# Optimization experiments

Measured on AMD Instinct MI355X. Metric: run time of the kernel, lower is better.

## Reference

```python
import jax, jax.numpy as jnp
import numpy as np

NUM_HEADS = 16
HEAD_DIM = 128
ROPE_BASE = 10000.0


def _rotate_half(x):
    x1, x2 = jnp.split(x, 2, axis=-1)
    return jnp.concatenate([-x2, x1], axis=-1)


def setup_inputs() -> dict:
    key = jax.random.key(0)
    ks = jax.random.split(key, 6)
    B, S, H = 2, 2048, 2048
    hidden_states = jax.random.normal(ks[0], (B, S, H), dtype=jnp.float32)
    # causal additive mask: 0 on/below diagonal, large negative above
    causal = jnp.tril(jnp.ones((S, S), dtype=bool))
    attention_mask = jnp.where(causal, 0.0, -1e9).astype(jnp.float32)[None, None]
    position_ids = jnp.broadcast_to(jnp.arange(S, dtype=jnp.int64), (B, S))
    sc = 1.0 / np.sqrt(H)
    Wq = jax.random.normal(ks[1], (H, H), dtype=jnp.float32) * sc
    Wk = jax.random.normal(ks[2], (H, H), dtype=jnp.float32) * sc
    Wv = jax.random.normal(ks[3], (H, H), dtype=jnp.float32) * sc
    Wo = jax.random.normal(ks[4], (H, H), dtype=jnp.float32) * sc
    return {"hidden_states": hidden_states, "attention_mask": attention_mask,
            "position_ids": position_ids, "Wq": Wq, "Wk": Wk, "Wv": Wv, "Wo": Wo}


def reference(hidden_states, attention_mask, position_ids, Wq, Wk, Wv, Wo):
    B, S, H = hidden_states.shape
    nH, hd = NUM_HEADS, HEAD_DIM
    # projections (torch Linear: x @ W.T)
    q = (hidden_states @ Wq.T).reshape(B, S, nH, hd).transpose(0, 2, 1, 3)  # [B,nH,S,hd]
    k = (hidden_states @ Wk.T).reshape(B, S, nH, hd).transpose(0, 2, 1, 3)
    v = (hidden_states @ Wv.T).reshape(B, S, nH, hd).transpose(0, 2, 1, 3)
    # rotary embeddings: cos/sin cache over positions, duplicated to full head_dim
    inv_freq = 1.0 / (ROPE_BASE ** (jnp.arange(0, hd, 2, dtype=jnp.float32) / hd))  # [hd/2]
    t = jnp.arange(S, dtype=jnp.float32)
    freqs = jnp.outer(t, inv_freq)                       # [S, hd/2]
    emb = jnp.concatenate([freqs, freqs], axis=-1)       # [S, hd]
    cos = jnp.cos(emb)[position_ids][:, None]            # [B,1,S,hd]
    sin = jnp.sin(emb)[position_ids][:, None]
    q = q * cos + _rotate_half(q) * sin
    k = k * cos + _rotate_half(k) * sin
    # eager attention
    scores = jnp.einsum('bhqd,bhkd->bhqk', q, k) / np.sqrt(hd).astype(np.float32)
    scores = scores + attention_mask
    attn = jax.nn.softmax(scores, axis=-1)
    out = jnp.einsum('bhqk,bhkd->bhqd', attn, v)         # [B,nH,S,hd]
    out = out.transpose(0, 2, 1, 3).reshape(B, S, H)
    return out @ Wo.T
```

## Files before the change

kernel.cpp:

```cpp
#include <hip/hip_runtime.h>
#include <cstdint>
#include <cstddef>

#define NH    16
#define HD    128
#define SEQ   2048
#define HID   2048
#define BATCH 2
#define MTOT  (BATCH*SEQ)

#define SCALE 0.08838834764831845f
#define L2E   1.4426950408889634f
#define KSCL  (0.08838834764831845f * 1.4426950408889634f)

typedef __bf16 bf16x8 __attribute__((ext_vector_type(8)));
typedef float  floatx4 __attribute__((ext_vector_type(4)));

__device__ __forceinline__ unsigned short f2bf(float f) {
  union { float f; unsigned u; } v; v.f = f;
  unsigned u = v.u;
  return (unsigned short)((u + 0x7FFFu + ((u >> 16) & 1u)) >> 16);
}
__device__ __forceinline__ float bf2f(unsigned short h) {
  union { unsigned u; float f; } v; v.u = ((unsigned)h) << 16; return v.f;
}

__device__ __forceinline__ void gld16(const unsigned short* g, unsigned short* l) {
  auto gp = reinterpret_cast<const __attribute__((address_space(1))) void*>(
      reinterpret_cast<uintptr_t>(g));
  auto lp = reinterpret_cast<__attribute__((address_space(3))) void*>(
      reinterpret_cast<uintptr_t>(l));
  __builtin_amdgcn_global_load_lds(gp, lp, 16, 0, 0);
}

__global__ void cvt_f32_bf16(const float* __restrict__ src,
                             unsigned short* __restrict__ dst, int n4) {
  int i = blockIdx.x * blockDim.x + threadIdx.x;
  if (i >= n4) return;
  float4 v = reinterpret_cast<const float4*>(src)[i];
  ushort4 o;
  o.x = f2bf(v.x); o.y = f2bf(v.y); o.z = f2bf(v.z); o.w = f2bf(v.w);
  reinterpret_cast<ushort4*>(dst)[i] = o;
}

__global__ void rope_table(float2* __restrict__ tab) {
  int idx = blockIdx.x * blockDim.x + threadIdx.x;
  if (idx >= SEQ * 64) return;
  int pos = idx >> 6, i = idx & 63;
  double freq = pow(10000.0, -(double)(2 * i) / 128.0);
  double th = (double)pos * freq;
  tab[idx] = make_float2((float)cos(th), (float)sin(th));
}

__global__ void rope_qk(unsigned short* __restrict__ Q,
                        unsigned short* __restrict__ Kk,
                        const float2* __restrict__ tab) {
  int idx = blockIdx.x * blockDim.x + threadIdx.x;
  if (idx >= BATCH * NH * SEQ * 64) return;
  int i  = idx & 63;
  int s  = (idx >> 6) & (SEQ - 1);
  int bh = idx >> 17;
  float2 cs = tab[s * 64 + i];
  size_t base = ((size_t)bh * SEQ + s) * HD;
  float qa = bf2f(Q[base + i]), qb = bf2f(Q[base + i + 64]);
  Q[base + i]      = f2bf(qa * cs.x - qb * cs.y);
  Q[base + i + 64] = f2bf(qb * cs.x + qa * cs.y);
  float ka = bf2f(Kk[base + i]), kb = bf2f(Kk[base + i + 64]);
  Kk[base + i]      = f2bf(ka * cs.x - kb * cs.y);
  Kk[base + i + 64] = f2bf(kb * cs.x + ka * cs.y);
}

__device__ __forceinline__ void gemm_core(const unsigned short* __restrict__ A,
                                          const unsigned short* __restrict__ B,
                                          int K, int mBase, int nBase,
                                          unsigned short* As, unsigned short* Bs,
                                          floatx4 acc[4][4]) {
  int tid  = threadIdx.x;
  int wave = tid >> 6, lane = tid & 63;
  int l16  = lane & 15, quad = lane >> 4;
  int wm   = wave >> 1, wn = wave & 1;

  const unsigned short* Ag = A + (size_t)mBase * K;
  const unsigned short* Bg = B + (size_t)nBase * K;

  for (int k0 = 0; k0 < K; k0 += 32) {
    __syncthreads();
#pragma unroll
    for (int r = 0; r < 2; ++r) {
      int row0 = wave * 32 + r * 16;
      int grow = row0 + (lane >> 2);
      int gcol = k0 + (lane & 3) * 8;
      gld16(Ag + (size_t)grow * K + gcol, As + row0 * 32 + lane * 8);
      gld16(Bg + (size_t)grow * K + gcol, Bs + row0 * 32 + lane * 8);
    }
    __syncthreads();

    bf16x8 af[4], bfr[4];
#pragma unroll
    for (int t = 0; t < 4; ++t) {
      af[t]  = *reinterpret_cast<const bf16x8*>(&As[(wm * 64 + t * 16 + l16) * 32 + quad * 8]);
      bfr[t] = *reinterpret_cast<const bf16x8*>(&Bs[(wn * 64 + t * 16 + l16) * 32 + quad * 8]);
    }
#pragma unroll
    for (int tm = 0; tm < 4; ++tm)
#pragma unroll
      for (int tn = 0; tn < 4; ++tn)
        acc[tm][tn] = __builtin_amdgcn_mfma_f32_16x16x32_bf16(af[tm], bfr[tn], acc[tm][tn], 0, 0, 0);
  }
}

__global__ __launch_bounds__(256)
void gemm_qkv(const unsigned short* __restrict__ Xb,
              const unsigned short* __restrict__ Wq,
              const unsigned short* __restrict__ Wk,
              const unsigned short* __restrict__ Wv,
              unsigned short* __restrict__ Qo,
              unsigned short* __restrict__ Ko,
              unsigned short* __restrict__ Vto) {
  __shared__ unsigned short As[128 * 32];
  __shared__ unsigned short Bs[128 * 32];
  int z = blockIdx.z;
  const unsigned short* W = (z == 0) ? Wq : (z == 1) ? Wk : Wv;
  int mBase = blockIdx.y * 128, nBase = blockIdx.x * 128;

  floatx4 acc[4][4];
#pragma unroll
  for (int i = 0; i < 4; ++i)
#pragma unroll
    for (int j = 0; j < 4; ++j) acc[i][j] = {0.f, 0.f, 0.f, 0.f};

  gemm_core(Xb, W, HID, mBase, nBase, As, Bs, acc);

  int tid = threadIdx.x;
  int wave = tid >> 6, lane = tid & 63;
  int l16 = lane & 15, quad = lane >> 4;
  int wm = wave >> 1, wn = wave & 1;

#pragma unroll
  for (int tm = 0; tm < 4; ++tm) {
    int mrow = mBase + wm * 64 + tm * 16 + quad * 4;
#pragma unroll
    for (int tn = 0; tn < 4; ++tn) {
      int n = nBase + wn * 64 + tn * 16 + l16;
      int hh = n >> 7, d = n & 127;
      if (z < 2) {
        unsigned short* dst = (z == 0) ? Qo : Ko;
#pragma unroll
        for (int r = 0; r < 4; ++r) {
          int m = mrow + r;
          int bb = m >> 11, s = m & (SEQ - 1);
          dst[(((size_t)bb * NH + hh) * SEQ + s) * HD + d] = f2bf(acc[tm][tn][r]);
        }
      } else {
        int bb = mrow >> 11, s = mrow & (SEQ - 1);
        ushort4 pk;
        pk.x = f2bf(acc[tm][tn][0]); pk.y = f2bf(acc[tm][tn][1]);
        pk.z = f2bf(acc[tm][tn][2]); pk.w = f2bf(acc[tm][tn][3]);
        *reinterpret_cast<ushort4*>(&Vto[(((size_t)bb * NH + hh) * HD + d) * SEQ + s]) = pk;
      }
    }
  }
}

__global__ __launch_bounds__(256)
void gemm_out(const unsigned short* __restrict__ Ob,
              const unsigned short* __restrict__ Wo,
              float* __restrict__ out) {
  __shared__ unsigned short As[128 * 32];
  __shared__ unsigned short Bs[128 * 32];
  int mBase = blockIdx.y * 128, nBase = blockIdx.x * 128;

  floatx4 acc[4][4];
#pragma unroll
  for (int i = 0; i < 4; ++i)
#pragma unroll
    for (int j = 0; j < 4; ++j) acc[i][j] = {0.f, 0.f, 0.f, 0.f};

  gemm_core(Ob, Wo, HID, mBase, nBase, As, Bs, acc);

  int tid = threadIdx.x;
  int wave = tid >> 6, lane = tid & 63;
  int l16 = lane & 15, quad = lane >> 4;
  int wm = wave >> 1, wn = wave & 1;

#pragma unroll
  for (int tm = 0; tm < 4; ++tm) {
    int mrow = mBase + wm * 64 + tm * 16 + quad * 4;
#pragma unroll
    for (int tn = 0; tn < 4; ++tn) {
      int n = nBase + wn * 64 + tn * 16 + l16;
#pragma unroll
      for (int r = 0; r < 4; ++r)
        out[(size_t)(mrow + r) * HID + n] = acc[tm][tn][r];
    }
  }
}

__global__ __launch_bounds__(256)
void attn_kernel(const unsigned short* __restrict__ Q,
                 const unsigned short* __restrict__ K,
                 const unsigned short* __restrict__ Vt,
                 unsigned short* __restrict__ Ob) {
  __shared__ unsigned short Ks[32 * 136];
  __shared__ unsigned short Vs[128 * 40];
  __shared__ unsigned short Ps[4][16 * 40];

  int qt = 31 - blockIdx.y;
  int bh = blockIdx.x;
  int b = bh >> 4, h = bh & 15;
  int q0 = qt * 64;
  int tid = threadIdx.x;
  int wave = tid >> 6, lane = tid & 63;
  int l16 = lane & 15, quad = lane >> 4;

  const size_t headQ = (size_t)bh * SEQ * HD;
  const size_t headV = (size_t)bh * HD * SEQ;

  bf16x8 qf[4];
  {
    int qrow = q0 + wave * 16 + l16;
    const unsigned short* qp = Q + headQ + (size_t)qrow * HD + quad * 8;
#pragma unroll
    for (int c = 0; c < 4; ++c)
      qf[c] = *reinterpret_cast<const bf16x8*>(qp + c * 32);
  }

  floatx4 oacc[8];
#pragma unroll
  for (int i = 0; i < 8; ++i) oacc[i] = {0.f, 0.f, 0.f, 0.f};
  float rs[4];
#pragma unroll
  for (int r = 0; r < 4; ++r) rs[r] = 0.f;

  int qq = q0 + wave * 16 + quad * 4;
  unsigned short* pw = Ps[wave];

  int nkt = q0 / 32 + 2;
  for (int kt = 0; kt < nkt; ++kt) {
    int k0 = kt * 32;
    __syncthreads();
#pragma unroll
    for (int rpt = 0; rpt < 2; ++rpt) {
      int c = tid + rpt * 256;
      int row = c >> 4, dc = (c & 15) * 8;
      *reinterpret_cast<uint4*>(&Ks[row * 136 + dc]) =
        *reinterpret_cast<const uint4*>(&K[headQ + (size_t)(k0 + row) * HD + dc]);
    }
#pragma unroll
    for (int rpt = 0; rpt < 2; ++rpt) {
      int c = tid + rpt * 256;
      int row = c >> 2, kc = (c & 3) * 8;
      *reinterpret_cast<uint4*>(&Vs[row * 40 + kc]) =
        *reinterpret_cast<const uint4*>(&Vt[headV + (size_t)row * SEQ + k0 + kc]);
    }
    __syncthreads();

    floatx4 sc[2];
#pragma unroll
    for (int nt = 0; nt < 2; ++nt) {
      floatx4 s4 = {0.f, 0.f, 0.f, 0.f};
#pragma unroll
      for (int c = 0; c < 4; ++c) {
        bf16x8 kf = *reinterpret_cast<const bf16x8*>(&Ks[(nt * 16 + l16) * 136 + c * 32 + quad * 8]);
        s4 = __builtin_amdgcn_mfma_f32_16x16x32_bf16(qf[c], kf, s4, 0, 0, 0);
      }
      sc[nt] = s4;
    }

#pragma unroll
    for (int nt = 0; nt < 2; ++nt) {
      int kk = k0 + nt * 16 + l16;
#pragma unroll
      for (int r = 0; r < 4; ++r) {
        float arg = (kk <= qq + r) ? fmaf(sc[nt][r], KSCL, -32.0f) : -1e9f;
        float p = exp2f(arg);
        rs[r] += p;
        pw[(quad * 4 + r) * 40 + nt * 16 + l16] = f2bf(p);
      }
    }
    __asm__ __volatile__("s_waitcnt lgkmcnt(0)" ::: "memory");
    bf16x8 pf = *reinterpret_cast<const bf16x8*>(&pw[l16 * 40 + quad * 8]);

#pragma unroll
    for (int dt = 0; dt < 8; ++dt) {
      bf16x8 vf = *reinterpret_cast<const bf16x8*>(&Vs[(dt * 16 + l16) * 40 + quad * 8]);
      oacc[dt] = __builtin_amdgcn_mfma_f32_16x16x32_bf16(pf, vf, oacc[dt], 0, 0, 0);
    }
  }

#pragma unroll
  for (int off = 1; off < 16; off <<= 1)
#pragma unroll
    for (int r = 0; r < 4; ++r) rs[r] += __shfl_xor(rs[r], off, 16);

  float inv[4];
#pragma unroll
  for (int r = 0; r < 4; ++r) inv[r] = 1.0f / rs[r];
#pragma unroll
  for (int dt = 0; dt < 8; ++dt)
#pragma unroll
    for (int r = 0; r < 4; ++r) {
      int s = q0 + wave * 16 + quad * 4 + r;
      Ob[(((size_t)b * SEQ + s) * NH + h) * HD + dt * 16 + l16] = f2bf(oacc[dt][r] * inv[r]);
    }
}

extern "C" void kernel_launch(void* const* d_in, const int* in_sizes, int n_in,
                              void* d_out, int out_size, void* d_ws, size_t ws_size,
                              hipStream_t stream) {
  const float* X  = (const float*)d_in[0];
  const float* Wq = (const float*)d_in[3];
  const float* Wk = (const float*)d_in[4];
  const float* Wv = (const float*)d_in[5];
  const float* Wo = (const float*)d_in[6];

  char* w = (char*)d_ws;
  size_t off = 0;
  auto alloc = [&](size_t bytes) { char* p = w + off; off += (bytes + 255) & ~(size_t)255; return p; };

  unsigned short* Xb  = (unsigned short*)alloc((size_t)MTOT * HID * 2);
  unsigned short* Wqb = (unsigned short*)alloc((size_t)HID * HID * 2);
  unsigned short* Wkb = (unsigned short*)alloc((size_t)HID * HID * 2);
  unsigned short* Wvb = (unsigned short*)alloc((size_t)HID * HID * 2);
  unsigned short* Wob = (unsigned short*)alloc((size_t)HID * HID * 2);
  unsigned short* Qb  = (unsigned short*)alloc((size_t)BATCH * NH * SEQ * HD * 2);
  unsigned short* Kb  = (unsigned short*)alloc((size_t)BATCH * NH * SEQ * HD * 2);
  unsigned short* Vtb = (unsigned short*)alloc((size_t)BATCH * NH * HD * SEQ * 2);
  unsigned short* Obf = (unsigned short*)alloc((size_t)BATCH * SEQ * NH * HD * 2);
  float2*         tab = (float2*)alloc((size_t)SEQ * 64 * sizeof(float2));

  const int nX4 = (MTOT * HID) / 4;
  const int nW4 = (HID * HID) / 4;
  cvt_f32_bf16<<<(nX4 + 255) / 256, 256, 0, stream>>>(X, Xb, nX4);
  cvt_f32_bf16<<<(nW4 + 255) / 256, 256, 0, stream>>>(Wq, Wqb, nW4);
  cvt_f32_bf16<<<(nW4 + 255) / 256, 256, 0, stream>>>(Wk, Wkb, nW4);
  cvt_f32_bf16<<<(nW4 + 255) / 256, 256, 0, stream>>>(Wv, Wvb, nW4);
  cvt_f32_bf16<<<(nW4 + 255) / 256, 256, 0, stream>>>(Wo, Wob, nW4);

  rope_table<<<(SEQ * 64 + 255) / 256, 256, 0, stream>>>(tab);

  gemm_qkv<<<dim3(HID / 128, MTOT / 128, 3), 256, 0, stream>>>(Xb, Wqb, Wkb, Wvb, Qb, Kb, Vtb);

  rope_qk<<<(BATCH * NH * SEQ * 64) / 256, 256, 0, stream>>>(Qb, Kb, tab);

  attn_kernel<<<dim3(BATCH * NH, SEQ / 64), 256, 0, stream>>>(Qb, Kb, Vtb, Obf);

  gemm_out<<<dim3(HID / 128, MTOT / 128), 256, 0, stream>>>(Obf, Wob, (float*)d_out);
}
```

Baseline: 423.8 us.

## Fuse RoPE into QKV GEMM epilogue and widen attention tiles to 128 queries

Rearranges which N columns each wave owns in the GEMM so that a lane holds both d and d+64 of the same head, then applies the rotary embedding directly in the QKV epilogue. This removes the separate rope_qk pass, which read and wrote Q and K a second time. Separately, the attention kernel now uses 512 threads covering 128 query rows, so each K/V tile staged in shared memory is reused by twice as many waves. Waves whose rows lie entirely above the diagonal skip the compute, at the cost of waiting at the barriers with nothing to do.

```diff
diff --git a/kernel.cpp b/kernel.cpp
--- a/kernel.cpp
+++ b/kernel.cpp
@@ -20,9 +20,6 @@
   union { float f; unsigned u; } v; v.f = f;
   unsigned u = v.u;
   return (unsigned short)((u + 0x7FFFu + ((u >> 16) & 1u)) >> 16);
-}
-__device__ __forceinline__ float bf2f(unsigned short h) {
-  union { unsigned u; float f; } v; v.u = ((unsigned)h) << 16; return v.f;
 }
 
 __device__ __forceinline__ void gld16(const unsigned short* g, unsigned short* l) {
@@ -52,22 +49,8 @@
   tab[idx] = make_float2((float)cos(th), (float)sin(th));
 }
 
-__global__ void rope_qk(unsigned short* __restrict__ Q,
-                        unsigned short* __restrict__ Kk,
-                        const float2* __restrict__ tab) {
-  int idx = blockIdx.x * blockDim.x + threadIdx.x;
-  if (idx >= BATCH * NH * SEQ * 64) return;
-  int i  = idx & 63;
-  int s  = (idx >> 6) & (SEQ - 1);
-  int bh = idx >> 17;
-  float2 cs = tab[s * 64 + i];
-  size_t base = ((size_t)bh * SEQ + s) * HD;
-  float qa = bf2f(Q[base + i]), qb = bf2f(Q[base + i + 64]);
-  Q[base + i]      = f2bf(qa * cs.x - qb * cs.y);
-  Q[base + i + 64] = f2bf(qb * cs.x + qa * cs.y);
-  float ka = bf2f(Kk[base + i]), kb = bf2f(Kk[base + i + 64]);
-  Kk[base + i]      = f2bf(ka * cs.x - kb * cs.y);
-  Kk[base + i + 64] = f2bf(kb * cs.x + ka * cs.y);
+__device__ __forceinline__ int noff(int wn, int t) {
+  return wn * 32 + (t & 1) * 16 + (t >> 1) * 64;
 }
 
 __device__ __forceinline__ void gemm_core(const unsigned short* __restrict__ A,
@@ -99,7 +82,7 @@
 #pragma unroll
     for (int t = 0; t < 4; ++t) {
       af[t]  = *reinterpret_cast<const bf16x8*>(&As[(wm * 64 + t * 16 + l16) * 32 + quad * 8]);
-      bfr[t] = *reinterpret_cast<const bf16x8*>(&Bs[(wn * 64 + t * 16 + l16) * 32 + quad * 8]);
+      bfr[t] = *reinterpret_cast<const bf16x8*>(&Bs[(noff(wn, t) + l16) * 32 + quad * 8]);
     }
 #pragma unroll
     for (int tm = 0; tm < 4; ++tm)
@@ -114,6 +97,7 @@
               const unsigned short* __restrict__ Wq,
               const unsigned short* __restrict__ Wk,
               const unsigned short* __restrict__ Wv,
+              const float2* __restrict__ tab,
               unsigned short* __restrict__ Qo,
               unsigned short* __restrict__ Ko,
               unsigned short* __restrict__ Vto) {
@@ -135,24 +119,32 @@
   int wave = tid >> 6, lane = tid & 63;
   int l16 = lane & 15, quad = lane >> 4;
   int wm = wave >> 1, wn = wave & 1;
+  int hh = nBase >> 7;
 
 #pragma unroll
   for (int tm = 0; tm < 4; ++tm) {
     int mrow = mBase + wm * 64 + tm * 16 + quad * 4;
-#pragma unroll
-    for (int tn = 0; tn < 4; ++tn) {
-      int n = nBase + wn * 64 + tn * 16 + l16;
-      int hh = n >> 7, d = n & 127;
-      if (z < 2) {
-        unsigned short* dst = (z == 0) ? Qo : Ko;
+    if (z < 2) {
+      unsigned short* dst = (z == 0) ? Qo : Ko;
+#pragma unroll
+      for (int p = 0; p < 2; ++p) {
+        int dlo = wn * 32 + p * 16 + l16;
 #pragma unroll
         for (int r = 0; r < 4; ++r) {
           int m = mrow + r;
           int bb = m >> 11, s = m & (SEQ - 1);
-          dst[(((size_t)bb * NH + hh) * SEQ + s) * HD + d] = f2bf(acc[tm][tn][r]);
+          float2 cs = tab[s * 64 + dlo];
+          float a = acc[tm][p][r], bv = acc[tm][p + 2][r];
+          size_t base = (((size_t)bb * NH + hh) * SEQ + s) * HD;
+          dst[base + dlo]      = f2bf(a * cs.x - bv * cs.y);
+          dst[base + dlo + 64] = f2bf(bv * cs.x + a * cs.y);
         }
-      } else {
-        int bb = mrow >> 11, s = mrow & (SEQ - 1);
+      }
+    } else {
+      int bb = mrow >> 11, s = mrow & (SEQ - 1);
+#pragma unroll
+      for (int tn = 0; tn < 4; ++tn) {
+        int d = noff(wn, tn) + l16;
         ushort4 pk;
         pk.x = f2bf(acc[tm][tn][0]); pk.y = f2bf(acc[tm][tn][1]);
         pk.z = f2bf(acc[tm][tn][2]); pk.w = f2bf(acc[tm][tn][3]);
@@ -188,7 +180,7 @@
     int mrow = mBase + wm * 64 + tm * 16 + quad * 4;
 #pragma unroll
     for (int tn = 0; tn < 4; ++tn) {
-      int n = nBase + wn * 64 + tn * 16 + l16;
+      int n = nBase + noff(wn, tn) + l16;
 #pragma unroll
       for (int r = 0; r < 4; ++r)
         out[(size_t)(mrow + r) * HID + n] = acc[tm][tn][r];
@@ -196,19 +188,19 @@
   }
 }
 
-__global__ __launch_bounds__(256)
+__global__ __launch_bounds__(512)
 void attn_kernel(const unsigned short* __restrict__ Q,
                  const unsigned short* __restrict__ K,
                  const unsigned short* __restrict__ Vt,
                  unsigned short* __restrict__ Ob) {
   __shared__ unsigned short Ks[32 * 136];
   __shared__ unsigned short Vs[128 * 40];
-  __shared__ unsigned short Ps[4][16 * 40];
-
-  int qt = 31 - blockIdx.y;
+  __shared__ unsigned short Ps[8][16 * 40];
+
+  int qt = 15 - blockIdx.y;
   int bh = blockIdx.x;
   int b = bh >> 4, h = bh & 15;
-  int q0 = qt * 64;
+  int q0 = qt * 128;
   int tid = threadIdx.x;
   int wave = tid >> 6, lane = tid & 63;
   int l16 = lane & 15, quad = lane >> 4;
@@ -233,58 +225,57 @@
   for (int r = 0; r < 4; ++r) rs[r] = 0.f;
 
   int qq = q0 + wave * 16 + quad * 4;
+  int qmax = q0 + wave * 16 + 15;
   unsigned short* pw = Ps[wave];
 
-  int nkt = q0 / 32 + 2;
+  int nkt = q0 / 32 + 4;
   for (int kt = 0; kt < nkt; ++kt) {
     int k0 = kt * 32;
     __syncthreads();
-#pragma unroll
-    for (int rpt = 0; rpt < 2; ++rpt) {
-      int c = tid + rpt * 256;
-      int row = c >> 4, dc = (c & 15) * 8;
+    {
+      int row = tid >> 4, dc = (tid & 15) * 8;
       *reinterpret_cast<uint4*>(&Ks[row * 136 + dc]) =
         *reinterpret_cast<const uint4*>(&K[headQ + (size_t)(k0 + row) * HD + dc]);
     }
-#pragma unroll
-    for (int rpt = 0; rpt < 2; ++rpt) {
-      int c = tid + rpt * 256;
-      int row = c >> 2, kc = (c & 3) * 8;
+    {
+      int row = tid >> 2, kc = (tid & 3) * 8;
       *reinterpret_cast<uint4*>(&Vs[row * 40 + kc]) =
         *reinterpret_cast<const uint4*>(&Vt[headV + (size_t)row * SEQ + k0 + kc]);
     }
     __syncthreads();
 
-    floatx4 sc[2];
-#pragma unroll
-    for (int nt = 0; nt < 2; ++nt) {
-      floatx4 s4 = {0.f, 0.f, 0.f, 0.f};
-#pragma unroll
-      for (int c = 0; c < 4; ++c) {
-        bf16x8 kf = *reinterpret_cast<const bf16x8*>(&Ks[(nt * 16 + l16) * 136 + c * 32 + quad * 8]);
-        s4 = __builtin_amdgcn_mfma_f32_16x16x32_bf16(qf[c], kf, s4, 0, 0, 0);
-      }
-      sc[nt] = s4;
-    }
-
-#pragma unroll
-    for (int nt = 0; nt < 2; ++nt) {
-      int kk = k0 + nt * 16 + l16;
-#pragma unroll
-      for (int r = 0; r < 4; ++r) {
-        float arg = (kk <= qq + r) ? fmaf(sc[nt][r], KSCL, -32.0f) : -1e9f;
-        float p = exp2f(arg);
-        rs[r] += p;
-        pw[(quad * 4 + r) * 40 + nt * 16 + l16] = f2bf(p);
-      }
-    }
-    __asm__ __volatile__("s_waitcnt lgkmcnt(0)" ::: "memory");
-    bf16x8 pf = *reinterpret_cast<const bf16x8*>(&pw[l16 * 40 + quad * 8]);
-
-#pragma unroll
-    for (int dt = 0; dt < 8; ++dt) {
-      bf16x8 vf = *reinterpret_cast<const bf16x8*>(&Vs[(dt * 16 + l16) * 40 + quad * 8]);
-      oacc[dt] = __builtin_amdgcn_mfma_f32_16x16x32_bf16(pf, vf, oacc[dt], 0, 0, 0);
+    if (k0 <= qmax) {
+      floatx4 sc[2];
+#pragma unroll
+      for (int nt = 0; nt < 2; ++nt) {
+        floatx4 s4 = {0.f, 0.f, 0.f, 0.f};
+#pragma unroll
+        for (int c = 0; c < 4; ++c) {
+          bf16x8 kf = *reinterpret_cast<const bf16x8*>(&Ks[(nt * 16 + l16) * 136 + c * 32 + quad * 8]);
+          s4 = __builtin_amdgcn_mfma_f32_16x16x32_bf16(qf[c], kf, s4, 0, 0, 0);
+        }
+        sc[nt] = s4;
+      }
+
+#pragma unroll
+      for (int nt = 0; nt < 2; ++nt) {
+        int kk = k0 + nt * 16 + l16;
+#pragma unroll
+        for (int r = 0; r < 4; ++r) {
+          float arg = (kk <= qq + r) ? fmaf(sc[nt][r], KSCL, -32.0f) : -1e9f;
+          float p = exp2f(arg);
+          rs[r] += p;
+          pw[(quad * 4 + r) * 40 + nt * 16 + l16] = f2bf(p);
+        }
+      }
+      __asm__ __volatile__("s_waitcnt lgkmcnt(0)" ::: "memory");
+      bf16x8 pf = *reinterpret_cast<const bf16x8*>(&pw[l16 * 40 + quad * 8]);
+
+#pragma unroll
+      for (int dt = 0; dt < 8; ++dt) {
+        bf16x8 vf = *reinterpret_cast<const bf16x8*>(&Vs[(dt * 16 + l16) * 40 + quad * 8]);
+        oacc[dt] = __builtin_amdgcn_mfma_f32_16x16x32_bf16(pf, vf, oacc[dt], 0, 0, 0);
+      }
     }
   }
 
@@ -331,19 +322,16 @@
 
   const int nX4 = (MTOT * HID) / 4;
   const int nW4 = (HID * HID) / 4;
+  rope_table<<<(SEQ * 64 + 255) / 256, 256, 0, stream>>>(tab);
   cvt_f32_bf16<<<(nX4 + 255) / 256, 256, 0, stream>>>(X, Xb, nX4);
   cvt_f32_bf16<<<(nW4 + 255) / 256, 256, 0, stream>>>(Wq, Wqb, nW4);
   cvt_f32_bf16<<<(nW4 + 255) / 256, 256, 0, stream>>>(Wk, Wkb, nW4);
   cvt_f32_bf16<<<(nW4 + 255) / 256, 256, 0, stream>>>(Wv, Wvb, nW4);
   cvt_f32_bf16<<<(nW4 + 255) / 256, 256, 0, stream>>>(Wo, Wob, nW4);
 
-  rope_table<<<(SEQ * 64 + 255) / 256, 256, 0, stream>>>(tab);
-
-  gemm_qkv<<<dim3(HID / 128, MTOT / 128, 3), 256, 0, stream>>>(Xb, Wqb, Wkb, Wvb, Qb, Kb, Vtb);
-
-  rope_qk<<<(BATCH * NH * SEQ * 64) / 256, 256, 0, stream>>>(Qb, Kb, tab);
-
-  attn_kernel<<<dim3(BATCH * NH, SEQ / 64), 256, 0, stream>>>(Qb, Kb, Vtb, Obf);
+  gemm_qkv<<<dim3(HID / 128, MTOT / 128, 3), 256, 0, stream>>>(Xb, Wqb, Wkb, Wvb, tab, Qb, Kb, Vtb);
+
+  attn_kernel<<<dim3(BATCH * NH, SEQ / 128), 512, 0, stream>>>(Qb, Kb, Vtb, Obf);
 
   gemm_out<<<dim3(HID / 128, MTOT / 128), 256, 0, stream>>>(Obf, Wob, (float*)d_out);
 }
```

Measured after the change: 439.9 us. +3.8%, slower.
